# Performance work log

Hardware: AMD Instinct MI355X
Metric: run time of the kernel (lower is better)

Reference implementation:

```python
import jax, jax.numpy as jnp
import numpy as np
import math

V, S, E, H, L, B = 50257, 1024, 768, 12, 12, 4
D = E // H
EPS = 1e-5


def setup_inputs() -> dict:
    key = jax.random.key(0)
    ks = jax.random.split(key, 20)
    sd = 0.02
    inp = {
        "idx": jax.random.randint(ks[0], (B, S), 0, V),
        "targets": jax.random.randint(ks[1], (B, S), 0, V),
        "wte": jax.random.normal(ks[2], (V, E), jnp.float32) * sd,  # tied with lm_head
        "wpe": jax.random.normal(ks[3], (S, E), jnp.float32) * sd,
        "ln1_g": jnp.ones((L, E), jnp.float32),
        "ln1_b": jnp.zeros((L, E), jnp.float32),
        "attn_w": jax.random.normal(ks[4], (L, E, 3 * E), jnp.float32) * sd,
        "attn_b": jnp.zeros((L, 3 * E), jnp.float32),
        "proj_w": jax.random.normal(ks[5], (L, E, E), jnp.float32) * (sd / math.sqrt(2 * L)),
        "proj_b": jnp.zeros((L, E), jnp.float32),
        "ln2_g": jnp.ones((L, E), jnp.float32),
        "ln2_b": jnp.zeros((L, E), jnp.float32),
        "fc_w": jax.random.normal(ks[6], (L, E, 4 * E), jnp.float32) * sd,
        "fc_b": jnp.zeros((L, 4 * E), jnp.float32),
        "fcp_w": jax.random.normal(ks[7], (L, 4 * E, E), jnp.float32) * (sd / math.sqrt(2 * L)),
        "fcp_b": jnp.zeros((L, E), jnp.float32),
        "lnf_g": jnp.ones((E,), jnp.float32),
        "lnf_b": jnp.zeros((E,), jnp.float32),
    }
    return inp


def layer_norm(x, g, b):
    mu = jnp.mean(x, axis=-1, keepdims=True)
    var = jnp.mean(jnp.square(x - mu), axis=-1, keepdims=True)
    return (x - mu) * jax.lax.rsqrt(var + EPS) * g + b


def reference(idx, targets, wte, wpe, ln1_g, ln1_b, attn_w, attn_b, proj_w, proj_b,
              ln2_g, ln2_b, fc_w, fc_b, fcp_w, fcp_b, lnf_g, lnf_b):
    seq = idx.shape[1]
    x = wte[idx] + wpe[:seq]  # [B,S,E]
    mask = jnp.tril(jnp.ones((seq, seq), bool))
    scale = 1.0 / math.sqrt(D)

    def block(x, p):
        l1g, l1b, aw, ab, pw, pb, l2g, l2b, fw, fb, fpw, fpb = p
        h = layer_norm(x, l1g, l1b)
        qkv = h @ aw + ab  # [B,S,3E]
        q, k, v = jnp.split(qkv, 3, axis=-1)
        q = q.reshape(-1, seq, H, D).transpose(0, 2, 1, 3)  # [B,H,S,D]
        k = k.reshape(-1, seq, H, D).transpose(0, 2, 1, 3)
        v = v.reshape(-1, seq, H, D).transpose(0, 2, 1, 3)
        scores = jnp.einsum('bhqd,bhkd->bhqk', q, k) * scale
        scores = jnp.where(mask, scores, -jnp.inf)
        attn = jax.nn.softmax(scores, axis=-1)
        y = jnp.einsum('bhqk,bhkd->bhqd', attn, v)
        y = y.transpose(0, 2, 1, 3).reshape(-1, seq, E)
        x = x + y @ pw + pb
        h2 = layer_norm(x, l2g, l2b)
        h2 = jax.nn.gelu(h2 @ fw + fb, approximate=False)
        x = x + h2 @ fpw + fpb
        return x, None

    x, _ = jax.lax.scan(block, x, (ln1_g, ln1_b, attn_w, attn_b, proj_w, proj_b,
                                   ln2_g, ln2_b, fc_w, fc_b, fcp_w, fcp_b))
    x = layer_norm(x, lnf_g, lnf_b)
    logits = x @ wte.T  # tied lm_head, [B,S,V]
    logp = jax.nn.log_softmax(logits, axis=-1)
    loss = -jnp.mean(jnp.take_along_axis(logp, targets[..., None], axis=-1))
    return logits, loss
```

## Files before the change

### kernel.cpp

```cpp
#include <hip/hip_runtime.h>
#include <hip/hip_bf16.h>
#include <math.h>

#define V 50257
#define SQ 1024
#define E 768
#define NH 12
#define NL 12
#define NB 4
#define MR (NB*SQ)

typedef __bf16 bf16x8 __attribute__((ext_vector_type(8)));
typedef float f32x4 __attribute__((ext_vector_type(4)));
typedef unsigned short us8 __attribute__((ext_vector_type(8)));

__device__ __forceinline__ float b2f(unsigned short u) {
    union { float f; unsigned int i; } x; x.i = ((unsigned int)u) << 16; return x.f;
}
__device__ __forceinline__ unsigned short f2b(float f) {
    unsigned int u = __float_as_uint(f);
    u = (u + 0x7fff + ((u >> 16) & 1)) >> 16;
    return (unsigned short)u;
}
__device__ __forceinline__ void gload16(const unsigned short* g, unsigned short* l) {
    __builtin_amdgcn_global_load_lds((const __attribute__((address_space(1))) void*)g,
                                     (__attribute__((address_space(3))) void*)l, 16, 0, 0);
}

__global__ __launch_bounds__(256)
void embed_k(const int* __restrict__ idx, const float* __restrict__ wte,
             const float* __restrict__ wpe, float* __restrict__ x)
{
    int r = blockIdx.x, t = threadIdx.x;
    int tok = idx[r];
    int s = r & (SQ - 1);
    const float* wt = wte + (size_t)tok * E;
    const float* wp = wpe + (size_t)s * E;
    float* xr = x + (size_t)r * E;
    for (int e = t; e < E; e += 256) xr[e] = wt[e] + wp[e];
}

__global__ __launch_bounds__(256)
void ln_k(const float* __restrict__ x, const float* __restrict__ g,
          const float* __restrict__ bb, unsigned short* __restrict__ out)
{
    int r = blockIdx.x, t = threadIdx.x;
    int lane = t & 63, wid = t >> 6;
    const float* xr = x + (size_t)r * E;
    float v0 = xr[t], v1 = xr[t + 256], v2 = xr[t + 512];
    float s = v0 + v1 + v2;
    #pragma unroll
    for (int o = 1; o < 64; o <<= 1) s += __shfl_xor(s, o);
    __shared__ float red[8];
    if (lane == 0) red[wid] = s;
    __syncthreads();
    float mu = (red[0] + red[1] + red[2] + red[3]) * (1.f / E);
    float d0 = v0 - mu, d1 = v1 - mu, d2 = v2 - mu;
    float s2 = d0 * d0 + d1 * d1 + d2 * d2;
    #pragma unroll
    for (int o = 1; o < 64; o <<= 1) s2 += __shfl_xor(s2, o);
    if (lane == 0) red[wid + 4] = s2;
    __syncthreads();
    float rs = rsqrtf((red[4] + red[5] + red[6] + red[7]) * (1.f / E) + 1e-5f);
    unsigned short* orow = out + (size_t)r * E;
    orow[t]       = f2b(d0 * rs * g[t] + bb[t]);
    orow[t + 256] = f2b(d1 * rs * g[t + 256] + bb[t + 256]);
    orow[t + 512] = f2b(d2 * rs * g[t + 512] + bb[t + 512]);
}

__global__ __launch_bounds__(256)
void conv_k(const float* __restrict__ in, unsigned short* __restrict__ out, int n4)
{
    int i = blockIdx.x * 256 + threadIdx.x;
    int stride = gridDim.x * 256;
    for (; i < n4; i += stride) {
        float4 v = ((const float4*)in)[i];
        ushort4 o;
        o.x = f2b(v.x); o.y = f2b(v.y); o.z = f2b(v.z); o.w = f2b(v.w);
        ((ushort4*)out)[i] = o;
    }
}

__global__ __launch_bounds__(256)
void tconv_k(const float* __restrict__ in, unsigned short* __restrict__ out, int Kd, int Nd)
{
    __shared__ float tile[32][33];
    int n0 = blockIdx.x * 32, k0 = blockIdx.y * 32;
    int tc = threadIdx.x & 31, tr = threadIdx.x >> 5;
    #pragma unroll
    for (int i = 0; i < 4; ++i)
        tile[tr + i * 8][tc] = in[(size_t)(k0 + tr + i * 8) * Nd + n0 + tc];
    __syncthreads();
    #pragma unroll
    for (int i = 0; i < 4; ++i)
        out[(size_t)(n0 + tr + i * 8) * Kd + k0 + tc] = f2b(tile[tc][tr + i * 8]);
}

template<int EPI>
__global__ __launch_bounds__(256)
void gemm_k(const unsigned short* __restrict__ A, const unsigned short* __restrict__ B,
            const float* __restrict__ bias, const float* __restrict__ resid,
            void* __restrict__ Cv, unsigned short* __restrict__ vt,
            float2* __restrict__ part, int M, int N, int K, int Nreal)
{
    __shared__ __align__(16) unsigned short As[128 * 64];
    __shared__ __align__(16) unsigned short Bs[128 * 64];
    const int t = threadIdx.x;
    const int lane = t & 63, wv = t >> 6;
    const int wr = wv >> 1, wc = wv & 1;
    const int m0 = blockIdx.x * 128, n0 = blockIdx.y * 128;
    const int lq = lane & 15, lg = lane >> 4;

    f32x4 acc[4][4];
    const f32x4 fz = {0.f, 0.f, 0.f, 0.f};
    #pragma unroll
    for (int i = 0; i < 4; ++i)
        #pragma unroll
        for (int j = 0; j < 4; ++j) acc[i][j] = fz;

    const int srow = t >> 3, sc = t & 7;

    for (int k0 = 0; k0 < K; k0 += 64) {
        #pragma unroll
        for (int i = 0; i < 4; ++i) {
            int row = srow + i * 32;
            int gc = ((sc ^ (row & 7)) << 3);
            gload16(A + (size_t)(m0 + row) * K + k0 + gc, &As[row * 64 + sc * 8]);
            int nrow = n0 + row;
            if (EPI == 3 && nrow >= Nreal) nrow = Nreal - 1;
            gload16(B + (size_t)nrow * K + k0 + gc, &Bs[row * 64 + sc * 8]);
        }
        __syncthreads();
        #pragma unroll
        for (int ks = 0; ks < 64; ks += 32) {
            bf16x8 af[4], bfr[4];
            #pragma unroll
            for (int mi = 0; mi < 4; ++mi) {
                int row = wr * 64 + mi * 16 + lq;
                int c = (ks >> 3) + lg;
                af[mi] = *(const bf16x8*)&As[row * 64 + ((c ^ (row & 7)) << 3)];
            }
            #pragma unroll
            for (int ni = 0; ni < 4; ++ni) {
                int row = wc * 64 + ni * 16 + lq;
                int c = (ks >> 3) + lg;
                bfr[ni] = *(const bf16x8*)&Bs[row * 64 + ((c ^ (row & 7)) << 3)];
            }
            #pragma unroll
            for (int mi = 0; mi < 4; ++mi)
                #pragma unroll
                for (int ni = 0; ni < 4; ++ni)
                    acc[mi][ni] = __builtin_amdgcn_mfma_f32_16x16x32_bf16(
                        af[mi], bfr[ni], acc[mi][ni], 0, 0, 0);
        }
        __syncthreads();
    }

    const int colb = n0 + wc * 64 + lq;
    const int rowb = m0 + wr * 64 + lg * 4;

    if constexpr (EPI == 3) {
        __shared__ float2 Ls[2][64][2];
        float* C = (float*)Cv;
        #pragma unroll
        for (int mi = 0; mi < 4; ++mi) {
            #pragma unroll
            for (int j = 0; j < 4; ++j) {
                int row = rowb + mi * 16 + j;
                float v[4];
                #pragma unroll
                for (int ni = 0; ni < 4; ++ni) {
                    int col = colb + ni * 16;
                    float vv = acc[mi][ni][j];
                    if (col < Nreal) C[(size_t)row * Nreal + col] = vv;
                    else vv = -1e30f;
                    v[ni] = vv;
                }
                float lm = fmaxf(fmaxf(v[0], v[1]), fmaxf(v[2], v[3]));
                #pragma unroll
                for (int o = 1; o < 16; o <<= 1) lm = fmaxf(lm, __shfl_xor(lm, o));
                float ls = __expf(v[0] - lm) + __expf(v[1] - lm)
                         + __expf(v[2] - lm) + __expf(v[3] - lm);
                #pragma unroll
                for (int o = 1; o < 16; o <<= 1) ls += __shfl_xor(ls, o);
                if (lq == 0) Ls[wr][mi * 16 + lg * 4 + j][wc] = make_float2(lm, ls);
            }
        }
        __syncthreads();
        if (t < 128) {
            float2 a = Ls[t >> 6][t & 63][0];
            float2 b = Ls[t >> 6][t & 63][1];
            float mm = fmaxf(a.x, b.x);
            float ss = a.y * __expf(a.x - mm) + b.y * __expf(b.x - mm);
            part[(size_t)blockIdx.y * MR + m0 + t] = make_float2(mm, ss);
        }
    } else if constexpr (EPI == 0) {
        unsigned short* C = (unsigned short*)Cv;
        #pragma unroll
        for (int mi = 0; mi < 4; ++mi) {
            int r0 = rowb + mi * 16;
            #pragma unroll
            for (int ni = 0; ni < 4; ++ni) {
                int col = colb + ni * 16;
                float b4 = bias[col];
                float vals[4];
                #pragma unroll
                for (int j = 0; j < 4; ++j) vals[j] = acc[mi][ni][j] + b4;
                #pragma unroll
                for (int j = 0; j < 4; ++j)
                    C[(size_t)(r0 + j) * N + col] = f2b(vals[j]);
                if (col >= 2 * E) {
                    int d = col - 2 * E; int hh = d >> 6; d &= 63;
                    int bb2 = r0 >> 10, kv = r0 & (SQ - 1);
                    unsigned int lo = (unsigned int)f2b(vals[0]) | ((unsigned int)f2b(vals[1]) << 16);
                    unsigned int hi = (unsigned int)f2b(vals[2]) | ((unsigned int)f2b(vals[3]) << 16);
                    uint2 u; u.x = lo; u.y = hi;
                    *(uint2*)&vt[(((size_t)bb2 * NH + hh) * 64 + d) * SQ + kv] = u;
                }
            }
        }
    } else {
        #pragma unroll
        for (int mi = 0; mi < 4; ++mi) {
            #pragma unroll
            for (int ni = 0; ni < 4; ++ni) {
                int col = colb + ni * 16;
                #pragma unroll
                for (int j = 0; j < 4; ++j) {
                    int row = rowb + mi * 16 + j;
                    float v = acc[mi][ni][j] + bias[col];
                    if constexpr (EPI == 1) {
                        ((float*)Cv)[(size_t)row * N + col] =
                            v + resid[(size_t)row * N + col];
                    } else {
                        float u = v + 0.044715f * v * v * v;
                        float e = __expf(-1.5957691216f * u);
                        v = v / (1.f + e);
                        ((unsigned short*)Cv)[(size_t)row * N + col] = f2b(v);
                    }
                }
            }
        }
    }
}

__global__ __launch_bounds__(256)
void attn_k(const unsigned short* __restrict__ qkv, const unsigned short* __restrict__ vtg,
            unsigned short* __restrict__ y)
{
    const int bid = blockIdx.x;
    const int qb  = (SQ / 64 - 1) - (bid / 48);
    const int bh  = bid % 48;
    const int h = bh % NH, b = bh / NH;
    const int t = threadIdx.x, lane = t & 63, wid = t >> 6;
    const int q0 = qb * 64;
    const int lq = lane & 15, lg = lane >> 4;

    __shared__ __align__(16) unsigned short Ks[64 * 72];
    __shared__ __align__(16) unsigned short Vs[64 * 72];
    __shared__ __align__(16) unsigned short Ps[4][16 * 72];

    const unsigned short* base  = qkv + (size_t)b * SQ * 2304;
    const unsigned short* vbase = vtg + (size_t)bh * 64 * SQ;

    const int qrow = q0 + wid * 16 + lq;
    bf16x8 qf0 = *(const bf16x8*)(base + (size_t)qrow * 2304 + h * 64 + lg * 8);
    bf16x8 qf1 = *(const bf16x8*)(base + (size_t)qrow * 2304 + h * 64 + 32 + lg * 8);

    const int sr = t >> 3, sc = t & 7;
    us8 ka, kb, va, vb;
    {
        const unsigned short* kp = base + (size_t)sr * 2304 + 768 + h * 64 + sc * 8;
        ka = *(const us8*)kp;
        kb = *(const us8*)(kp + (size_t)32 * 2304);
        const unsigned short* vp = vbase + (size_t)sr * SQ + sc * 8;
        va = *(const us8*)vp;
        vb = *(const us8*)(vp + (size_t)32 * SQ);
    }

    f32x4 of[4];
    const f32x4 fz = {0.f, 0.f, 0.f, 0.f};
    #pragma unroll
    for (int i = 0; i < 4; ++i) of[i] = fz;
    float mreg = -1e30f, lreg = 0.f;

    for (int tt = 0; tt <= qb; ++tt) {
        __syncthreads();
        *(us8*)&Ks[sr * 72 + sc * 8] = ka;
        *(us8*)&Ks[(sr + 32) * 72 + sc * 8] = kb;
        *(us8*)&Vs[sr * 72 + sc * 8] = va;
        *(us8*)&Vs[(sr + 32) * 72 + sc * 8] = vb;
        __syncthreads();
        if (tt < qb) {
            int kv0n = (tt + 1) * 64;
            const unsigned short* kp = base + (size_t)(kv0n + sr) * 2304 + 768 + h * 64 + sc * 8;
            ka = *(const us8*)kp;
            kb = *(const us8*)(kp + (size_t)32 * 2304);
            const unsigned short* vp = vbase + (size_t)sr * SQ + kv0n + sc * 8;
            va = *(const us8*)vp;
            vb = *(const us8*)(vp + (size_t)32 * SQ);
        }

        f32x4 sf[4];
        #pragma unroll
        for (int mi = 0; mi < 4; ++mi) sf[mi] = fz;
        #pragma unroll
        for (int mi = 0; mi < 4; ++mi) {
            const unsigned short* kr = &Ks[(mi * 16 + lq) * 72 + lg * 8];
            bf16x8 k0 = *(const bf16x8*)kr;
            bf16x8 k1 = *(const bf16x8*)(kr + 32);
            sf[mi] = __builtin_amdgcn_mfma_f32_16x16x32_bf16(k0, qf0, sf[mi], 0, 0, 0);
            sf[mi] = __builtin_amdgcn_mfma_f32_16x16x32_bf16(k1, qf1, sf[mi], 0, 0, 0);
        }

        float pv[16];
        const int kvb = tt * 64 + lg * 4;
        #pragma unroll
        for (int mi = 0; mi < 4; ++mi)
            #pragma unroll
            for (int j = 0; j < 4; ++j) {
                float s = sf[mi][j] * 0.125f;
                if (tt == qb && (kvb + mi * 16 + j) > qrow) s = -1e30f;
                pv[mi * 4 + j] = s;
            }
        float tm = pv[0];
        #pragma unroll
        for (int i = 1; i < 16; ++i) tm = fmaxf(tm, pv[i]);
        tm = fmaxf(tm, __shfl_xor(tm, 16));
        tm = fmaxf(tm, __shfl_xor(tm, 32));
        float mn  = fmaxf(mreg, tm);
        float fac = __expf(mreg - mn);
        float ts = 0.f;
        #pragma unroll
        for (int i = 0; i < 16; ++i) { float p = __expf(pv[i] - mn); pv[i] = p; ts += p; }
        ts += __shfl_xor(ts, 16);
        ts += __shfl_xor(ts, 32);
        lreg = lreg * fac + ts;
        mreg = mn;
        #pragma unroll
        for (int j = 0; j < 4; ++j) {
            float fj = __shfl(fac, 20 * lg + j);
            of[0][j] *= fj; of[1][j] *= fj; of[2][j] *= fj; of[3][j] *= fj;
        }
        unsigned short* pw = &Ps[wid][lq * 72];
        #pragma unroll
        for (int mi = 0; mi < 4; ++mi) {
            unsigned int lo = (unsigned int)f2b(pv[mi * 4 + 0]) | ((unsigned int)f2b(pv[mi * 4 + 1]) << 16);
            unsigned int hi = (unsigned int)f2b(pv[mi * 4 + 2]) | ((unsigned int)f2b(pv[mi * 4 + 3]) << 16);
            uint2 u; u.x = lo; u.y = hi;
            *(uint2*)&pw[mi * 16 + lg * 4] = u;
        }
        #pragma unroll
        for (int ks = 0; ks < 2; ++ks) {
            bf16x8 pf = *(const bf16x8*)&Ps[wid][lq * 72 + ks * 32 + lg * 8];
            #pragma unroll
            for (int ni = 0; ni < 4; ++ni) {
                bf16x8 vf = *(const bf16x8*)&Vs[(ni * 16 + lq) * 72 + ks * 32 + lg * 8];
                of[ni] = __builtin_amdgcn_mfma_f32_16x16x32_bf16(pf, vf, of[ni], 0, 0, 0);
            }
        }
    }

    float inv = 1.f / lreg;
    #pragma unroll
    for (int j = 0; j < 4; ++j) {
        float fj = __shfl(inv, 20 * lg + j);
        int row = q0 + wid * 16 + lg * 4 + j;
        unsigned short* yr = y + ((size_t)b * SQ + row) * E + h * 64 + lq;
        #pragma unroll
        for (int ni = 0; ni < 4; ++ni)
            yr[ni * 16] = f2b(of[ni][j] * fj);
    }
}

__global__ __launch_bounds__(256)
void lossred_k(const float2* __restrict__ part, const float* __restrict__ logits,
               const int* __restrict__ tgt, float* __restrict__ rl, int NT)
{
    int t = threadIdx.x, lane = t & 63, wid = t >> 6;
    int r = blockIdx.x * 4 + wid;
    float m = -1e30f, s = 0.f;
    for (int nt = lane; nt < NT; nt += 64) {
        float2 p = part[(size_t)nt * MR + r];
        float mm = fmaxf(m, p.x);
        s = s * __expf(m - mm) + p.y * __expf(p.x - mm);
        m = mm;
    }
    #pragma unroll
    for (int o = 1; o < 64; o <<= 1) {
        float m2 = __shfl_xor(m, o), s2 = __shfl_xor(s, o);
        float mm = fmaxf(m, m2);
        s = s * __expf(m - mm) + s2 * __expf(m2 - mm);
        m = mm;
    }
    if (lane == 0)
        rl[r] = __logf(s) + m - logits[(size_t)r * V + tgt[r]];
}

__global__ __launch_bounds__(256)
void finloss_k(const float* __restrict__ rl, float* __restrict__ out)
{
    __shared__ float red[256];
    int t = threadIdx.x;
    float s = 0.f;
    for (int i = t; i < MR; i += 256) s += rl[i];
    red[t] = s; __syncthreads();
    for (int o = 128; o > 0; o >>= 1) { if (t < o) red[t] += red[t + o]; __syncthreads(); }
    if (t == 0) out[0] = red[0] * (1.f / MR);
}

extern "C" void kernel_launch(void* const* d_in, const int* in_sizes, int n_in,
                              void* d_out, int out_size, void* d_ws, size_t ws_size,
                              hipStream_t stream)
{
    const int*   idx    = (const int*)  d_in[0];
    const int*   tgt    = (const int*)  d_in[1];
    const float* wte    = (const float*)d_in[2];
    const float* wpe    = (const float*)d_in[3];
    const float* ln1_g  = (const float*)d_in[4];
    const float* ln1_b  = (const float*)d_in[5];
    const float* attn_w = (const float*)d_in[6];
    const float* attn_b = (const float*)d_in[7];
    const float* proj_w = (const float*)d_in[8];
    const float* proj_b = (const float*)d_in[9];
    const float* ln2_g  = (const float*)d_in[10];
    const float* ln2_b  = (const float*)d_in[11];
    const float* fc_w   = (const float*)d_in[12];
    const float* fc_b   = (const float*)d_in[13];
    const float* fcp_w  = (const float*)d_in[14];
    const float* fcp_b  = (const float*)d_in[15];
    const float* lnf_g  = (const float*)d_in[16];
    const float* lnf_b  = (const float*)d_in[17];

    unsigned char* p = (unsigned char*)d_ws;
    auto alloc = [&](size_t bytes) {
        unsigned char* r = p; p += (bytes + 255) & ~(size_t)255; return r;
    };
    float*          x    = (float*)         alloc((size_t)MR * E * 4);
    unsigned short* h    = (unsigned short*)alloc((size_t)MR * E * 2);
    unsigned short* qkv  = (unsigned short*)alloc((size_t)MR * 3 * E * 2);
    unsigned short* yb   = (unsigned short*)alloc((size_t)MR * E * 2);
    unsigned short* act  = (unsigned short*)alloc((size_t)MR * 4 * E * 2);
    unsigned short* wq   = (unsigned short*)alloc((size_t)3 * E * E * 2);
    unsigned short* wp   = (unsigned short*)alloc((size_t)E * E * 2);
    unsigned short* wf   = (unsigned short*)alloc((size_t)4 * E * E * 2);
    unsigned short* wfp  = (unsigned short*)alloc((size_t)4 * E * E * 2);
    unsigned short* wteb = (unsigned short*)alloc((size_t)V * E * 2);
    unsigned short* vtg  = (unsigned short*)alloc((size_t)NB * NH * 64 * SQ * 2);
    float2*         part = (float2*)        alloc((size_t)393 * MR * 8);
    float*          rl   = (float*)         alloc((size_t)MR * 4);

    float* logits = (float*)d_out;
    float* lossp  = logits + (size_t)MR * V;

    embed_k<<<MR, 256, 0, stream>>>(idx, wte, wpe, x);
    conv_k<<<2048, 256, 0, stream>>>(wte, wteb, (int)((size_t)V * E / 4));

    for (int l = 0; l < NL; ++l) {
        tconv_k<<<dim3(3 * E / 32, E / 32), 256, 0, stream>>>(
            attn_w + (size_t)l * E * 3 * E, wq, E, 3 * E);
        tconv_k<<<dim3(E / 32, E / 32), 256, 0, stream>>>(
            proj_w + (size_t)l * E * E, wp, E, E);
        tconv_k<<<dim3(4 * E / 32, E / 32), 256, 0, stream>>>(
            fc_w + (size_t)l * E * 4 * E, wf, E, 4 * E);
        tconv_k<<<dim3(E / 32, 4 * E / 32), 256, 0, stream>>>(
            fcp_w + (size_t)l * 4 * E * E, wfp, 4 * E, E);

        ln_k<<<MR, 256, 0, stream>>>(x, ln1_g + l * E, ln1_b + l * E, h);
        gemm_k<0><<<dim3(32, 18), 256, 0, stream>>>(
            h, wq, attn_b + (size_t)l * 3 * E, nullptr, qkv, vtg, nullptr,
            MR, 3 * E, E, 3 * E);
        attn_k<<<768, 256, 0, stream>>>(qkv, vtg, yb);
        gemm_k<1><<<dim3(32, 6), 256, 0, stream>>>(
            yb, wp, proj_b + (size_t)l * E, x, x, nullptr, nullptr, MR, E, E, E);
        ln_k<<<MR, 256, 0, stream>>>(x, ln2_g + l * E, ln2_b + l * E, h);
        gemm_k<2><<<dim3(32, 24), 256, 0, stream>>>(
            h, wf, fc_b + (size_t)l * 4 * E, nullptr, act, nullptr, nullptr,
            MR, 4 * E, E, 4 * E);
        gemm_k<1><<<dim3(32, 6), 256, 0, stream>>>(
            act, wfp, fcp_b + (size_t)l * E, x, x, nullptr, nullptr, MR, E, 4 * E, E);
    }

    ln_k<<<MR, 256, 0, stream>>>(x, lnf_g, lnf_b, h);
    gemm_k<3><<<dim3(32, 393), 256, 0, stream>>>(
        h, wteb, nullptr, nullptr, logits, nullptr, part, MR, 50304, E, V);

    lossred_k<<<MR / 4, 256, 0, stream>>>(part, logits, tgt, rl, 393);
    finloss_k<<<1, 256, 0, stream>>>(rl, lossp);
}
```

Before: 3.126 ms.

## Double-buffer GEMM shared tiles and batch weight conversion across layers

The GEMM kernel now uses two shared-memory buffers for the A and B tiles and issues the loads for the next K tile before computing on the current one, with one barrier per iteration instead of two. Separately, when the workspace is large enough, all twelve layers' weights are transposed and converted to bf16 up front in four 3D-grid launches instead of 48 small per-layer launches. The double buffer doubles LDS use to 64 KB per block, which may reduce occupancy. Pre-converting every layer needs extra workspace and falls back to per-layer conversion if that space is not available.

```diff
diff --git a/kernel.cpp b/kernel.cpp
--- a/kernel.cpp
+++ b/kernel.cpp
@@ -85,6 +85,9 @@
 void tconv_k(const float* __restrict__ in, unsigned short* __restrict__ out, int Kd, int Nd)
 {
     __shared__ float tile[32][33];
+    size_t loff = (size_t)blockIdx.z * Kd * Nd;
+    in  += loff;
+    out += loff;
     int n0 = blockIdx.x * 32, k0 = blockIdx.y * 32;
     int tc = threadIdx.x & 31, tr = threadIdx.x >> 5;
     #pragma unroll
@@ -103,8 +106,8 @@
             void* __restrict__ Cv, unsigned short* __restrict__ vt,
             float2* __restrict__ part, int M, int N, int K, int Nreal)
 {
-    __shared__ __align__(16) unsigned short As[128 * 64];
-    __shared__ __align__(16) unsigned short Bs[128 * 64];
+    __shared__ __align__(16) unsigned short As[2][128 * 64];
+    __shared__ __align__(16) unsigned short Bs[2][128 * 64];
     const int t = threadIdx.x;
     const int lane = t & 63, wv = t >> 6;
     const int wr = wv >> 1, wc = wv & 1;
@@ -120,17 +123,25 @@
 
     const int srow = t >> 3, sc = t & 7;
 
-    for (int k0 = 0; k0 < K; k0 += 64) {
+    auto stage = [&](int buf, int k0) {
         #pragma unroll
         for (int i = 0; i < 4; ++i) {
             int row = srow + i * 32;
             int gc = ((sc ^ (row & 7)) << 3);
-            gload16(A + (size_t)(m0 + row) * K + k0 + gc, &As[row * 64 + sc * 8]);
+            gload16(A + (size_t)(m0 + row) * K + k0 + gc, &As[buf][row * 64 + sc * 8]);
             int nrow = n0 + row;
             if (EPI == 3 && nrow >= Nreal) nrow = Nreal - 1;
-            gload16(B + (size_t)nrow * K + k0 + gc, &Bs[row * 64 + sc * 8]);
-        }
-        __syncthreads();
+            gload16(B + (size_t)nrow * K + k0 + gc, &Bs[buf][row * 64 + sc * 8]);
+        }
+    };
+
+    stage(0, 0);
+    __syncthreads();
+
+    const int KT = K >> 6;
+    int cur = 0;
+    for (int kt = 0; kt < KT; ++kt) {
+        if (kt + 1 < KT) stage(cur ^ 1, (kt + 1) << 6);
         #pragma unroll
         for (int ks = 0; ks < 64; ks += 32) {
             bf16x8 af[4], bfr[4];
@@ -138,13 +149,13 @@
             for (int mi = 0; mi < 4; ++mi) {
                 int row = wr * 64 + mi * 16 + lq;
                 int c = (ks >> 3) + lg;
-                af[mi] = *(const bf16x8*)&As[row * 64 + ((c ^ (row & 7)) << 3)];
+                af[mi] = *(const bf16x8*)&As[cur][row * 64 + ((c ^ (row & 7)) << 3)];
             }
             #pragma unroll
             for (int ni = 0; ni < 4; ++ni) {
                 int row = wc * 64 + ni * 16 + lq;
                 int c = (ks >> 3) + lg;
-                bfr[ni] = *(const bf16x8*)&Bs[row * 64 + ((c ^ (row & 7)) << 3)];
+                bfr[ni] = *(const bf16x8*)&Bs[cur][row * 64 + ((c ^ (row & 7)) << 3)];
             }
             #pragma unroll
             for (int mi = 0; mi < 4; ++mi)
@@ -154,6 +165,7 @@
                         af[mi], bfr[ni], acc[mi][ni], 0, 0, 0);
         }
         __syncthreads();
+        cur ^= 1;
     }
 
     const int colb = n0 + wc * 64 + lq;
@@ -441,30 +453,48 @@
     unsigned short* qkv  = (unsigned short*)alloc((size_t)MR * 3 * E * 2);
     unsigned short* yb   = (unsigned short*)alloc((size_t)MR * E * 2);
     unsigned short* act  = (unsigned short*)alloc((size_t)MR * 4 * E * 2);
-    unsigned short* wq   = (unsigned short*)alloc((size_t)3 * E * E * 2);
-    unsigned short* wp   = (unsigned short*)alloc((size_t)E * E * 2);
-    unsigned short* wf   = (unsigned short*)alloc((size_t)4 * E * E * 2);
-    unsigned short* wfp  = (unsigned short*)alloc((size_t)4 * E * E * 2);
     unsigned short* wteb = (unsigned short*)alloc((size_t)V * E * 2);
     unsigned short* vtg  = (unsigned short*)alloc((size_t)NB * NH * 64 * SQ * 2);
     float2*         part = (float2*)        alloc((size_t)393 * MR * 8);
     float*          rl   = (float*)         alloc((size_t)MR * 4);
 
+    size_t used = (size_t)(p - (unsigned char*)d_ws);
+    size_t perL = (size_t)12 * E * E * 2 + 4 * 256;
+    int NLW = (ws_size >= used + (size_t)NL * perL) ? NL : 1;
+    unsigned short* wqA  = (unsigned short*)alloc((size_t)NLW * 3 * E * E * 2);
+    unsigned short* wpA  = (unsigned short*)alloc((size_t)NLW * E * E * 2);
+    unsigned short* wfA  = (unsigned short*)alloc((size_t)NLW * 4 * E * E * 2);
+    unsigned short* wfpA = (unsigned short*)alloc((size_t)NLW * 4 * E * E * 2);
+
     float* logits = (float*)d_out;
     float* lossp  = logits + (size_t)MR * V;
 
     embed_k<<<MR, 256, 0, stream>>>(idx, wte, wpe, x);
     conv_k<<<2048, 256, 0, stream>>>(wte, wteb, (int)((size_t)V * E / 4));
 
+    if (NLW == NL) {
+        tconv_k<<<dim3(3 * E / 32, E / 32, NL), 256, 0, stream>>>(attn_w, wqA, E, 3 * E);
+        tconv_k<<<dim3(E / 32, E / 32, NL), 256, 0, stream>>>(proj_w, wpA, E, E);
+        tconv_k<<<dim3(4 * E / 32, E / 32, NL), 256, 0, stream>>>(fc_w, wfA, E, 4 * E);
+        tconv_k<<<dim3(E / 32, 4 * E / 32, NL), 256, 0, stream>>>(fcp_w, wfpA, 4 * E, E);
+    }
+
     for (int l = 0; l < NL; ++l) {
-        tconv_k<<<dim3(3 * E / 32, E / 32), 256, 0, stream>>>(
-            attn_w + (size_t)l * E * 3 * E, wq, E, 3 * E);
-        tconv_k<<<dim3(E / 32, E / 32), 256, 0, stream>>>(
-            proj_w + (size_t)l * E * E, wp, E, E);
-        tconv_k<<<dim3(4 * E / 32, E / 32), 256, 0, stream>>>(
-            fc_w + (size_t)l * E * 4 * E, wf, E, 4 * E);
-        tconv_k<<<dim3(E / 32, 4 * E / 32), 256, 0, stream>>>(
-            fcp_w + (size_t)l * 4 * E * E, wfp, 4 * E, E);
+        int lw = (NLW == NL) ? l : 0;
+        unsigned short* wq  = wqA  + (size_t)lw * 3 * E * E;
+        unsigned short* wp  = wpA  + (size_t)lw * E * E;
+        unsigned short* wf  = wfA  + (size_t)lw * 4 * E * E;
+        unsigned short* wfp = wfpA + (size_t)lw * 4 * E * E;
+        if (NLW != NL) {
+            tconv_k<<<dim3(3 * E / 32, E / 32), 256, 0, stream>>>(
+                attn_w + (size_t)l * E * 3 * E, wq, E, 3 * E);
+            tconv_k<<<dim3(E / 32, E / 32), 256, 0, stream>>>(
+                proj_w + (size_t)l * E * E, wp, E, E);
+            tconv_k<<<dim3(4 * E / 32, E / 32), 256, 0, stream>>>(
+                fc_w + (size_t)l * E * 4 * E, wf, E, 4 * E);
+            tconv_k<<<dim3(E / 32, 4 * E / 32), 256, 0, stream>>>(
+                fcp_w + (size_t)l * 4 * E * E, wfp, 4 * E, E);
+        }
 
         ln_k<<<MR, 256, 0, stream>>>(x, ln1_g + l * E, ln1_b + l * E, h);
         gemm_k<0><<<dim3(32, 18), 256, 0, stream>>>(
```

New measurement: 3.326 ms. 6.4% more time.
